# Optimization experiments

Measured on AMD Instinct MI355X. Metric: run time of the kernel, lower is better.

Reference implementation:

```python
import jax, jax.numpy as jnp
import numpy as np

ALPHA = 0.5
NUM_NB = 8


def setup_inputs() -> dict:
    key = jax.random.key(0)
    k1, k2 = jax.random.split(key)
    pc1 = jax.random.normal(k1, (4, 3, 8192), dtype=jnp.float32)
    pred_flow = jax.random.normal(k2, (4, 3, 8192), dtype=jnp.float32)
    return {"pc1": pc1, "pred_flow": pred_flow}


def reference(pc1, pred_flow):
    # pc1, pred_flow: [B, 3, N] -> [B, N, 3]
    B, _, N = pc1.shape
    k = NUM_NB
    p = jnp.transpose(pc1, (0, 2, 1))         # [B, N, 3]
    f = jnp.transpose(pred_flow, (0, 2, 1))   # [B, N, 3]

    sq = jnp.sum(p * p, axis=-1)
    sqrdist = sq[:, :, None] + sq[:, None, :] - 2.0 * jnp.einsum('bnd,bmd->bnm', p, p)

    # k+1 smallest (sorted ascending), drop self (first column)
    neg_d, kidx = jax.lax.top_k(-sqrdist, k + 1)  # descending in -d == ascending in d
    dists = -neg_d[:, :, 1:]                      # [B, N, k]
    kidx = kidx[:, :, 1:]                         # [B, N, k]
    dists = jnp.maximum(dists, 0.0)

    # softmax over all N*k weights per batch
    w = jax.nn.softmax(jnp.exp(-dists / ALPHA).reshape(B, N * k), axis=1)
    w = w.reshape(B, N, k)

    # gather neighbor flows: [B, N, k, 3]
    grouped = jnp.take_along_axis(f[:, None, :, :],
                                  kidx[:, :, :, None],
                                  axis=2)
    diff = jnp.linalg.norm(grouped - f[:, :, None, :], axis=3)  # [B, N, k]
    diff_flow = (N * w * diff).sum(axis=2)                      # [B, N]
    return jnp.mean(diff_flow)
```

## Files before the change

### kernel.cpp

```cpp
#include <hip/hip_runtime.h>
#include <hip/hip_bf16.h>
#include <math.h>

#define BATCH 4
#define NQ 8192
#define KNB 8
#define K1 9
#define TILE 1024
#define CAP 25
#define THSAMP 256
#define SPART 2
#define IDXMASK 8191u
#define KEYMASK 0xFFFFE000u

#define CHAIN9(KEY) { unsigned kk = (KEY); \
  _Pragma("unroll") \
  for (int j = 0; j < K1; ++j) { \
    unsigned lo = min(kk, nk[j]); unsigned hi = max(kk, nk[j]); \
    nk[j] = lo; kk = hi; } }

#define DRAIN() { \
  for (int i = 0; i < cnt; ++i) { \
    unsigned key = sbuf[base + i]; \
    if (key < nk[K1-1]) CHAIN9(key); \
  } \
  cnt = 0; \
  thetaU = min(thetaU, nk[K1-1] | 0x1FFFu); }

#define GPROC(VX, VY, VZ, CIDX) { \
  float dx = qx - (VX); float dy = qy - (VY); float dz = qz - (VZ); \
  float d = dx*dx + dy*dy + dz*dz; \
  unsigned du = __float_as_uint(d); \
  sbuf[base + cnt] = (du & KEYMASK) | (unsigned)(CIDX); \
  cnt += (du <= thetaU) ? 1 : 0; }

__global__ __launch_bounds__(256) void theta_kernel(
    const float* __restrict__ pc, unsigned* __restrict__ thetaOut)
{
  __shared__ float swx[THSAMP], swy[THSAMP], swz[THSAMP];
  const int b = blockIdx.y, p = blockIdx.z;
  const int q = blockIdx.x * 256 + threadIdx.x;
  const float* __restrict__ px = pc + (size_t)b * 3 * NQ;
  const float* __restrict__ py = px + NQ;
  const float* __restrict__ pz = px + 2 * NQ;
  const int tid = threadIdx.x;
  const int si = tid * (NQ / THSAMP) + p * (NQ / THSAMP / SPART);
  swx[tid] = px[si]; swy[tid] = py[si]; swz[tid] = pz[si];
  __syncthreads();
  const float qx = px[q], qy = py[q], qz = pz[q];
  unsigned nk[K1];
#pragma unroll
  for (int j = 0; j < K1; ++j) nk[j] = 0xFFFFFFFFu;
  for (int i = 0; i < THSAMP; ++i) {
    float dx = qx - swx[i], dy = qy - swy[i], dz = qz - swz[i];
    float d = dx * dx + dy * dy + dz * dz;
    CHAIN9(__float_as_uint(d));
  }
  thetaOut[(size_t)(b * NQ + q) * SPART + p] = nk[K1 - 1] | 0x1FFFu;
}

__global__ __launch_bounds__(256) void knn_kernel(
    const float* __restrict__ pc, const unsigned* __restrict__ thetaIn,
    unsigned* __restrict__ wsK, int P, int cpp)
{
  __shared__ float sx[TILE], sy[TILE], sz[TILE];
  __shared__ unsigned sbuf[256 * CAP];
  const int b = blockIdx.y;
  const int p = blockIdx.z;
  const int q = blockIdx.x * 256 + threadIdx.x;
  const float* __restrict__ px = pc + (size_t)b * 3 * NQ;
  const float* __restrict__ py = px + NQ;
  const float* __restrict__ pz = px + 2 * NQ;
  const float qx = px[q], qy = py[q], qz = pz[q];

  uint2 th = ((const uint2*)thetaIn)[b * NQ + q];
  unsigned thetaU = min(th.x, th.y);

  unsigned nk[K1];
#pragma unroll
  for (int j = 0; j < K1; ++j) nk[j] = 0xFFFFFFFFu;

  const unsigned base = (unsigned)threadIdx.x * CAP;
  int cnt = 0;
  const int c0 = p * cpp;

  for (int t0 = 0; t0 < cpp; t0 += TILE) {
    __syncthreads();
    {
      const float4* gx = (const float4*)(px + c0 + t0);
      const float4* gy = (const float4*)(py + c0 + t0);
      const float4* gz = (const float4*)(pz + c0 + t0);
      float4* lx = (float4*)sx; float4* ly = (float4*)sy; float4* lz = (float4*)sz;
      for (int i = threadIdx.x; i < TILE / 4; i += 256) {
        lx[i] = gx[i]; ly[i] = gy[i]; lz[i] = gz[i];
      }
    }
    __syncthreads();

    const float4* sx4 = (const float4*)sx;
    const float4* sy4 = (const float4*)sy;
    const float4* sz4 = (const float4*)sz;
    for (int i4 = 0; i4 < TILE / 4; i4 += 2) {
      if (__any(cnt >= CAP - 8)) { DRAIN(); }
      float4 vx = sx4[i4], vy = sy4[i4], vz = sz4[i4];
      int cb = c0 + t0 + i4 * 4;
      GPROC(vx.x, vy.x, vz.x, cb + 0);
      GPROC(vx.y, vy.y, vz.y, cb + 1);
      GPROC(vx.z, vy.z, vz.z, cb + 2);
      GPROC(vx.w, vy.w, vz.w, cb + 3);
      vx = sx4[i4 + 1]; vy = sy4[i4 + 1]; vz = sz4[i4 + 1];
      GPROC(vx.x, vy.x, vz.x, cb + 4);
      GPROC(vx.y, vy.y, vz.y, cb + 5);
      GPROC(vx.z, vy.z, vz.z, cb + 6);
      GPROC(vx.w, vy.w, vz.w, cb + 7);
    }
  }
  DRAIN();

  size_t o = ((size_t)((b * NQ + q) * P + p)) * K1;
#pragma unroll
  for (int j = 0; j < K1; ++j) wsK[o + j] = nk[j];
}

__global__ __launch_bounds__(256) void loss_kernel(
    const float* __restrict__ pc, const float* __restrict__ pf,
    const unsigned* __restrict__ wsK, float* __restrict__ acc, int P)
{
  const int b = blockIdx.y;
  const int q = blockIdx.x * 256 + threadIdx.x;
  const float* __restrict__ px = pc + (size_t)b * 3 * NQ;
  const float* __restrict__ py = px + NQ;
  const float* __restrict__ pz = px + 2 * NQ;
  const float* __restrict__ fx = pf + (size_t)b * 3 * NQ;
  const float* __restrict__ fy = fx + NQ;
  const float* __restrict__ fz = fx + 2 * NQ;

  unsigned nk[KNB];
#pragma unroll
  for (int j = 0; j < KNB; ++j) nk[j] = 0xFFFFFFFFu;

  const size_t o = (size_t)((b * NQ + q) * P) * K1;
  const int total = P * K1;
  for (int m = 0; m < total; ++m) {
    unsigned key = wsK[o + m];
    if ((key & IDXMASK) == (unsigned)q) continue;
    if (key < nk[KNB - 1]) {
      unsigned kk = key;
#pragma unroll
      for (int j = 0; j < KNB; ++j) {
        unsigned lo = min(kk, nk[j]); unsigned hi = max(kk, nk[j]);
        nk[j] = lo; kk = hi;
      }
    }
  }

  const float qx = px[q], qy = py[q], qz = pz[q];
  const float fqx = fx[q], fqy = fy[q], fqz = fz[q];
  float ssum = 0.f, sdsum = 0.f;
#pragma unroll
  for (int j = 0; j < KNB; ++j) {
    int i = (int)(nk[j] & IDXMASK);
    float dx = qx - px[i], dy = qy - py[i], dz = qz - pz[i];
    float d = dx * dx + dy * dy + dz * dz;
    float e = expf(expf(-2.0f * d));
    float gx = fx[i] - fqx, gy = fy[i] - fqy, gz = fz[i] - fqz;
    float diff = sqrtf(gx * gx + gy * gy + gz * gz);
    ssum += e; sdsum += e * diff;
  }

  for (int off = 32; off > 0; off >>= 1) {
    ssum += __shfl_down(ssum, off);
    sdsum += __shfl_down(sdsum, off);
  }
  __shared__ float r[8];
  const int lane = threadIdx.x & 63, wid = threadIdx.x >> 6;
  if (lane == 0) { r[wid * 2] = ssum; r[wid * 2 + 1] = sdsum; }
  __syncthreads();
  if (threadIdx.x == 0) {
    float s0 = r[0] + r[2] + r[4] + r[6];
    float s1 = r[1] + r[3] + r[5] + r[7];
    atomicAdd(&acc[b * 2 + 0], s0);
    atomicAdd(&acc[b * 2 + 1], s1);
  }
}

__global__ void final_kernel(const float* __restrict__ acc, float* __restrict__ out)
{
  if (threadIdx.x == 0) {
    float s = 0.f;
    for (int b = 0; b < BATCH; ++b) s += acc[b * 2 + 1] / acc[b * 2];
    out[0] = s * (1.0f / BATCH);
  }
}

extern "C" void kernel_launch(void* const* d_in, const int* in_sizes, int n_in,
                              void* d_out, int out_size, void* d_ws, size_t ws_size,
                              hipStream_t stream) {
  const float* pc = (const float*)d_in[0];
  const float* pf = (const float*)d_in[1];
  float* out = (float*)d_out;
  float* acc = (float*)d_ws;
  unsigned* thetaBuf = (unsigned*)((char*)d_ws + 256);
  const size_t thetaBytes = (size_t)BATCH * NQ * SPART * sizeof(unsigned);
  unsigned* wsK = (unsigned*)((char*)d_ws + 256 + thetaBytes);

  const size_t needP8 = 256 + thetaBytes + (size_t)BATCH * NQ * 8 * K1 * sizeof(unsigned);
  const size_t needP4 = 256 + thetaBytes + (size_t)BATCH * NQ * 4 * K1 * sizeof(unsigned);
  const int P = (ws_size >= needP8) ? 8 : ((ws_size >= needP4) ? 4 : 1);
  const int cpp = NQ / P;

  hipMemsetAsync(d_ws, 0, 256, stream);

  dim3 g0(NQ / 256, BATCH, SPART);
  theta_kernel<<<g0, 256, 0, stream>>>(pc, thetaBuf);

  dim3 g1(NQ / 256, BATCH, P);
  knn_kernel<<<g1, 256, 0, stream>>>(pc, thetaBuf, wsK, P, cpp);

  dim3 g2(NQ / 256, BATCH);
  loss_kernel<<<g2, 256, 0, stream>>>(pc, pf, wsK, acc, P);

  final_kernel<<<1, 64, 0, stream>>>(acc, out);
}
```

Before: 153.6 us.

## Filter kNN candidates with precomputed half-norm dot-product score and 16-bit indices

```diff
diff --git a/kernel.cpp b/kernel.cpp
--- a/kernel.cpp
+++ b/kernel.cpp
@@ -7,11 +7,12 @@
 #define KNB 8
 #define K1 9
 #define TILE 1024
-#define CAP 25
+#define CAP 24
 #define THSAMP 256
 #define SPART 2
 #define IDXMASK 8191u
 #define KEYMASK 0xFFFFE000u
+#define EPS_S 1e-3f
 
 #define CHAIN9(KEY) { unsigned kk = (KEY); \
   _Pragma("unroll") \
@@ -19,23 +20,26 @@
     unsigned lo = min(kk, nk[j]); unsigned hi = max(kk, nk[j]); \
     nk[j] = lo; kk = hi; } }
 
-#define DRAIN() { \
+#define DRAIN(T0) { \
   for (int i = 0; i < cnt; ++i) { \
-    unsigned key = sbuf[base + i]; \
+    int j = sbuf[base + i]; \
+    float dx = qx - sx[j], dy = qy - sy[j], dz = qz - sz[j]; \
+    float d = dx*dx + dy*dy + dz*dz; \
+    unsigned key = (__float_as_uint(d) & KEYMASK) | (unsigned)(c0 + (T0) + j); \
     if (key < nk[K1-1]) CHAIN9(key); \
   } \
   cnt = 0; \
-  thetaU = min(thetaU, nk[K1-1] | 0x1FFFu); }
-
-#define GPROC(VX, VY, VZ, CIDX) { \
-  float dx = qx - (VX); float dy = qy - (VY); float dz = qz - (VZ); \
-  float d = dx*dx + dy*dy + dz*dz; \
-  unsigned du = __float_as_uint(d); \
-  sbuf[base + cnt] = (du & KEYMASK) | (unsigned)(CIDX); \
-  cnt += (du <= thetaU) ? 1 : 0; }
+  if (nk[K1-1] != 0xFFFFFFFFu) { \
+    float td = __uint_as_float(nk[K1-1] | 0x1FFFu); \
+    thetaS = fminf(thetaS, 0.5f*(td - qq) + EPS_S); \
+  } }
+
+#define GPROC(SS, JLOCAL) { \
+  if ((SS) <= thetaS) { sbuf[base + cnt] = (unsigned short)(JLOCAL); cnt++; } }
 
 __global__ __launch_bounds__(256) void theta_kernel(
-    const float* __restrict__ pc, unsigned* __restrict__ thetaOut)
+    const float* __restrict__ pc, unsigned* __restrict__ thetaOut,
+    float* __restrict__ hOut)
 {
   __shared__ float swx[THSAMP], swy[THSAMP], swz[THSAMP];
   const int b = blockIdx.y, p = blockIdx.z;
@@ -48,6 +52,7 @@
   swx[tid] = px[si]; swy[tid] = py[si]; swz[tid] = pz[si];
   __syncthreads();
   const float qx = px[q], qy = py[q], qz = pz[q];
+  if (p == 0) hOut[b * NQ + q] = 0.5f * (qx*qx + qy*qy + qz*qz);
   unsigned nk[K1];
 #pragma unroll
   for (int j = 0; j < K1; ++j) nk[j] = 0xFFFFFFFFu;
@@ -60,21 +65,25 @@
 }
 
 __global__ __launch_bounds__(256) void knn_kernel(
-    const float* __restrict__ pc, const unsigned* __restrict__ thetaIn,
-    unsigned* __restrict__ wsK, int P, int cpp)
-{
-  __shared__ float sx[TILE], sy[TILE], sz[TILE];
-  __shared__ unsigned sbuf[256 * CAP];
+    const float* __restrict__ pc, const float* __restrict__ hB,
+    const unsigned* __restrict__ thetaIn, unsigned* __restrict__ wsK,
+    int P, int cpp)
+{
+  __shared__ float sx[TILE], sy[TILE], sz[TILE], sh[TILE];
+  __shared__ unsigned short sbuf[256 * CAP];
   const int b = blockIdx.y;
   const int p = blockIdx.z;
   const int q = blockIdx.x * 256 + threadIdx.x;
   const float* __restrict__ px = pc + (size_t)b * 3 * NQ;
   const float* __restrict__ py = px + NQ;
   const float* __restrict__ pz = px + 2 * NQ;
+  const float* __restrict__ ph = hB + (size_t)b * NQ;
   const float qx = px[q], qy = py[q], qz = pz[q];
+  const float nqx = -qx, nqy = -qy, nqz = -qz;
+  const float qq = qx*qx + qy*qy + qz*qz;
 
   uint2 th = ((const uint2*)thetaIn)[b * NQ + q];
-  unsigned thetaU = min(th.x, th.y);
+  float thetaS = 0.5f * (__uint_as_float(min(th.x, th.y)) - qq) + EPS_S;
 
   unsigned nk[K1];
 #pragma unroll
@@ -90,9 +99,11 @@
       const float4* gx = (const float4*)(px + c0 + t0);
       const float4* gy = (const float4*)(py + c0 + t0);
       const float4* gz = (const float4*)(pz + c0 + t0);
-      float4* lx = (float4*)sx; float4* ly = (float4*)sy; float4* lz = (float4*)sz;
+      const float4* gh = (const float4*)(ph + c0 + t0);
+      float4* lx = (float4*)sx; float4* ly = (float4*)sy;
+      float4* lz = (float4*)sz; float4* lh = (float4*)sh;
       for (int i = threadIdx.x; i < TILE / 4; i += 256) {
-        lx[i] = gx[i]; ly[i] = gy[i]; lz[i] = gz[i];
+        lx[i] = gx[i]; ly[i] = gy[i]; lz[i] = gz[i]; lh[i] = gh[i];
       }
     }
     __syncthreads();
@@ -100,22 +111,27 @@
     const float4* sx4 = (const float4*)sx;
     const float4* sy4 = (const float4*)sy;
     const float4* sz4 = (const float4*)sz;
+    const float4* sh4 = (const float4*)sh;
     for (int i4 = 0; i4 < TILE / 4; i4 += 2) {
-      if (__any(cnt >= CAP - 8)) { DRAIN(); }
-      float4 vx = sx4[i4], vy = sy4[i4], vz = sz4[i4];
-      int cb = c0 + t0 + i4 * 4;
-      GPROC(vx.x, vy.x, vz.x, cb + 0);
-      GPROC(vx.y, vy.y, vz.y, cb + 1);
-      GPROC(vx.z, vy.z, vz.z, cb + 2);
-      GPROC(vx.w, vy.w, vz.w, cb + 3);
-      vx = sx4[i4 + 1]; vy = sy4[i4 + 1]; vz = sz4[i4 + 1];
-      GPROC(vx.x, vy.x, vz.x, cb + 4);
-      GPROC(vx.y, vy.y, vz.y, cb + 5);
-      GPROC(vx.z, vy.z, vz.z, cb + 6);
-      GPROC(vx.w, vy.w, vz.w, cb + 7);
+      if (__any(cnt >= CAP - 8)) { DRAIN(t0); }
+      float4 X = sx4[i4], Y = sy4[i4], Z = sz4[i4], H = sh4[i4];
+      const int jb = i4 * 4;
+      float s0 = fmaf(nqx, X.x, fmaf(nqy, Y.x, fmaf(nqz, Z.x, H.x)));
+      float s1 = fmaf(nqx, X.y, fmaf(nqy, Y.y, fmaf(nqz, Z.y, H.y)));
+      float s2 = fmaf(nqx, X.z, fmaf(nqy, Y.z, fmaf(nqz, Z.z, H.z)));
+      float s3 = fmaf(nqx, X.w, fmaf(nqy, Y.w, fmaf(nqz, Z.w, H.w)));
+      GPROC(s0, jb + 0); GPROC(s1, jb + 1);
+      GPROC(s2, jb + 2); GPROC(s3, jb + 3);
+      X = sx4[i4 + 1]; Y = sy4[i4 + 1]; Z = sz4[i4 + 1]; H = sh4[i4 + 1];
+      float s4 = fmaf(nqx, X.x, fmaf(nqy, Y.x, fmaf(nqz, Z.x, H.x)));
+      float s5 = fmaf(nqx, X.y, fmaf(nqy, Y.y, fmaf(nqz, Z.y, H.y)));
+      float s6 = fmaf(nqx, X.z, fmaf(nqy, Y.z, fmaf(nqz, Z.z, H.z)));
+      float s7 = fmaf(nqx, X.w, fmaf(nqy, Y.w, fmaf(nqz, Z.w, H.w)));
+      GPROC(s4, jb + 4); GPROC(s5, jb + 5);
+      GPROC(s6, jb + 6); GPROC(s7, jb + 7);
     }
-  }
-  DRAIN();
+    DRAIN(t0);
+  }
 
   size_t o = ((size_t)((b * NQ + q) * P + p)) * K1;
 #pragma unroll
@@ -200,22 +216,25 @@
   const float* pf = (const float*)d_in[1];
   float* out = (float*)d_out;
   float* acc = (float*)d_ws;
+  const size_t thetaBytes = (size_t)BATCH * NQ * SPART * sizeof(unsigned);
+  const size_t hBytes = (size_t)BATCH * NQ * sizeof(float);
   unsigned* thetaBuf = (unsigned*)((char*)d_ws + 256);
-  const size_t thetaBytes = (size_t)BATCH * NQ * SPART * sizeof(unsigned);
-  unsigned* wsK = (unsigned*)((char*)d_ws + 256 + thetaBytes);
-
-  const size_t needP8 = 256 + thetaBytes + (size_t)BATCH * NQ * 8 * K1 * sizeof(unsigned);
-  const size_t needP4 = 256 + thetaBytes + (size_t)BATCH * NQ * 4 * K1 * sizeof(unsigned);
+  float* hBuf = (float*)((char*)d_ws + 256 + thetaBytes);
+  unsigned* wsK = (unsigned*)((char*)d_ws + 256 + thetaBytes + hBytes);
+
+  const size_t fixed = 256 + thetaBytes + hBytes;
+  const size_t needP8 = fixed + (size_t)BATCH * NQ * 8 * K1 * sizeof(unsigned);
+  const size_t needP4 = fixed + (size_t)BATCH * NQ * 4 * K1 * sizeof(unsigned);
   const int P = (ws_size >= needP8) ? 8 : ((ws_size >= needP4) ? 4 : 1);
   const int cpp = NQ / P;
 
   hipMemsetAsync(d_ws, 0, 256, stream);
 
   dim3 g0(NQ / 256, BATCH, SPART);
-  theta_kernel<<<g0, 256, 0, stream>>>(pc, thetaBuf);
+  theta_kernel<<<g0, 256, 0, stream>>>(pc, thetaBuf, hBuf);
 
   dim3 g1(NQ / 256, BATCH, P);
-  knn_kernel<<<g1, 256, 0, stream>>>(pc, thetaBuf, wsK, P, cpp);
+  knn_kernel<<<g1, 256, 0, stream>>>(pc, hBuf, thetaBuf, wsK, P, cpp);
 
   dim3 g2(NQ / 256, BATCH);
   loss_kernel<<<g2, 256, 0, stream>>>(pc, pf, wsK, acc, P);
```

New measurement: 134.3 us. -12.5%, faster.
